# Kernel optimization log

Measured on AMD Instinct MI355X. Metric: run time of the kernel, lower is better.

## Reference

```python
import jax, jax.numpy as jnp
import numpy as np

E = 640000
N_AGENTS = 50000
D = 128
NUM_S = 50000


def setup_inputs() -> dict:
    key = jax.random.key(0)
    k1, k2, k3 = jax.random.split(key, 3)
    edge_weights = jax.random.uniform(k1, (E,), dtype=jnp.float32)
    agent_features = jax.random.normal(k2, (N_AGENTS, D), dtype=jnp.float32)
    edge_index = jax.random.randint(k3, (2, E), 0, NUM_S, dtype=jnp.int64)
    return {
        "edge_weights": edge_weights,
        "agent_features": agent_features,
        "edge_index": edge_index,
        "num_s": NUM_S,
    }


def reference(edge_weights, agent_features, edge_index, num_s):
    s_idx = edge_index[0]
    a_idx = edge_index[1]
    # gather per-edge agent features: [E, D]
    eaf = agent_features[a_idx]
    # weighted scatter-add: per-source feature sums [num_s, D] and weight sums [num_s]
    sum_wf = jax.ops.segment_sum(edge_weights[:, None] * eaf, s_idx, num_segments=num_s)
    sum_w = jax.ops.segment_sum(edge_weights, s_idx, num_segments=num_s)
    mean_per_s = sum_wf / (sum_w[:, None] + 1e-8)
    # second pass: weighted squared deviation per edge, scattered per source
    sq_diff = jnp.sum((eaf - mean_per_s[s_idx]) ** 2, axis=1)  # [E]
    var_per_s = jax.ops.segment_sum(edge_weights * sq_diff, s_idx, num_segments=num_s)
    valid = sum_w > 0
    n_valid = jnp.sum(valid)
    loss = jnp.sum(jnp.where(valid, var_per_s, 0.0)) / jnp.maximum(n_valid, 1).astype(var_per_s.dtype)
    return jnp.where(n_valid > 0, loss, jnp.asarray(0.0, var_per_s.dtype))
```

## Files before the change

### kernel.cpp

```cpp
#include <hip/hip_runtime.h>
#include <hip/hip_fp16.h>


#define D  128
#define NS 50000
#define KMAX 64
#define NBINS 391
#define BINB 512
#define CAP_PB 24

typedef unsigned long long ull;
typedef float f32x2 __attribute__((ext_vector_type(2)));


__global__ __launch_bounds__(256) void prep_bin(
    const float* __restrict__ af, unsigned char* __restrict__ af_q,
    float* __restrict__ sqnorm, float* __restrict__ accum, int* __restrict__ done,
    const int* __restrict__ s_idx, const int* __restrict__ a_idx,
    const float* __restrict__ ew,
    unsigned* __restrict__ blkCnt,
    ull* __restrict__ coarse,
    int E, int num_a)
{
    __shared__ unsigned hist[NBINS];
    const int tid = threadIdx.x;

    if (blockIdx.x < BINB) {
        const int b     = blockIdx.x;
        const int chunk = (E + BINB - 1) / BINB;
        const int e0    = b * chunk;
        const int e1    = min(E, e0 + chunk);

        for (int t = tid; t < NBINS; t += 256) hist[t] = 0;
        __syncthreads();
        for (int i = e0 + tid; i < e1; i += 256)
            atomicAdd(&hist[(unsigned)s_idx[i] >> 7], 1u);
        __syncthreads();
        for (int t = tid; t < NBINS; t += 256) {
            blkCnt[t * BINB + b] = min(hist[t], (unsigned)CAP_PB);
            hist[t] = 0;
        }
        __syncthreads();
        for (int i = e0 + tid; i < e1; i += 256) {
            int s = s_idx[i];
            unsigned bin = (unsigned)s >> 7;
            unsigned r   = atomicAdd(&hist[bin], 1u);
            if (r < CAP_PB) {
                unsigned low = ((unsigned)a_idx[i] << 16)
                             | (unsigned)__half_as_ushort(__float2half(ew[i]));
                coarse[((size_t)bin * BINB + b) * CAP_PB + r] =
                    ((ull)((unsigned)s & 127u) << 32) | (ull)low;
            }
        }
    } else {
        int pb     = blockIdx.x - BINB;
        int gtid   = pb * 256 + tid;
        int stride = ((int)gridDim.x - BINB) * 256;
        if (gtid == 0) { accum[0] = 0.f; accum[1] = 0.f; *done = 0; }

        for (int u = gtid; u < num_a * 16; u += stride) {
            int a    = u >> 4;
            int comp = (u & 15) << 3;
            const float* src = af + (size_t)a * D + comp;
            float4 v0 = *reinterpret_cast<const float4*>(src);
            float4 v1 = *reinterpret_cast<const float4*>(src + 4);
            unsigned lo = __builtin_amdgcn_cvt_pk_fp8_f32(v0.x, v0.y, 0u, false);
            lo = __builtin_amdgcn_cvt_pk_fp8_f32(v0.z, v0.w, lo, true);
            unsigned hi = __builtin_amdgcn_cvt_pk_fp8_f32(v1.x, v1.y, 0u, false);
            hi = __builtin_amdgcn_cvt_pk_fp8_f32(v1.z, v1.w, hi, true);
            int p  = comp >> 6;
            int cc = comp & 63;
            *reinterpret_cast<ull*>(af_q + ((size_t)p * num_a + a) * 64 + cc) =
                ((ull)hi << 32) | (ull)lo;

            f32x2 q0 = __builtin_amdgcn_cvt_pk_f32_fp8(lo, false);
            f32x2 q1 = __builtin_amdgcn_cvt_pk_f32_fp8(lo, true);
            f32x2 q2 = __builtin_amdgcn_cvt_pk_f32_fp8(hi, false);
            f32x2 q3 = __builtin_amdgcn_cvt_pk_f32_fp8(hi, true);
            float ss = q0.x*q0.x + q0.y*q0.y + q1.x*q1.x + q1.y*q1.y
                     + q2.x*q2.x + q2.y*q2.y + q3.x*q3.x + q3.y*q3.y;
            #pragma unroll
            for (int m = 1; m <= 8; m <<= 1) ss += __shfl_xor(ss, m, 64);
            if ((u & 15) == 0) sqnorm[a] = ss;
        }
    }
}


__global__ __launch_bounds__(256) void final_bucket(
    const ull* __restrict__ coarse,
    const unsigned* __restrict__ blkCnt,
    unsigned* __restrict__ bucket, int* __restrict__ cnt, int num_s)
{
    __shared__ unsigned lcnt[128];
    int bin = blockIdx.x;
    int tid = threadIdx.x;
    if (tid < 128) lcnt[tid] = 0;
    __syncthreads();
    for (int rr = tid; rr < BINB; rr += 256) {
        unsigned c = blkCnt[bin * BINB + rr];
        const ull* reg = coarse + ((size_t)bin * BINB + rr) * CAP_PB;
        for (unsigned r = 0; r < c; ++r) {
            ull e = reg[r];
            unsigned s7 = (unsigned)(e >> 32);
            unsigned k  = atomicAdd(&lcnt[s7], 1u);
            if (k < KMAX) {
                int s = bin * 128 + (int)s7;
                bucket[((size_t)s << 6) + k] = (unsigned)e;
            }
        }
    }
    __syncthreads();
    if (tid < 128) {
        int s = bin * 128 + tid;
        if (s < num_s) cnt[s] = (int)min(lcnt[tid], (unsigned)KMAX);
    }
}

__device__ __forceinline__ void fma16(const uint4& x, float w, float* acc) {
    f32x2 t;
    t = __builtin_amdgcn_cvt_pk_f32_fp8(x.x, false); acc[0]  += w*t.x; acc[1]  += w*t.y;
    t = __builtin_amdgcn_cvt_pk_f32_fp8(x.x, true);  acc[2]  += w*t.x; acc[3]  += w*t.y;
    t = __builtin_amdgcn_cvt_pk_f32_fp8(x.y, false); acc[4]  += w*t.x; acc[5]  += w*t.y;
    t = __builtin_amdgcn_cvt_pk_f32_fp8(x.y, true);  acc[6]  += w*t.x; acc[7]  += w*t.y;
    t = __builtin_amdgcn_cvt_pk_f32_fp8(x.z, false); acc[8]  += w*t.x; acc[9]  += w*t.y;
    t = __builtin_amdgcn_cvt_pk_f32_fp8(x.z, true);  acc[10] += w*t.x; acc[11] += w*t.y;
    t = __builtin_amdgcn_cvt_pk_f32_fp8(x.w, false); acc[12] += w*t.x; acc[13] += w*t.y;
    t = __builtin_amdgcn_cvt_pk_f32_fp8(x.w, true);  acc[14] += w*t.x; acc[15] += w*t.y;
}

__device__ __forceinline__ float decw(unsigned wa) {
    return __half2float(__ushort_as_half((unsigned short)(wa & 0xFFFFu)));
}


__global__ __launch_bounds__(256) void slice_merged(
    const unsigned char* __restrict__ af_q,
    const float* __restrict__ sqnorm,
    const unsigned* __restrict__ bucket,
    const int* __restrict__ cnt,
    float* __restrict__ fn2a, float* __restrict__ fn2b,
    float* __restrict__ s2acc, float* __restrict__ wsumv,
    int num_s, int num_a)
{
    const bool p0  = (blockIdx.x & 1u) == 0u;
    const unsigned char* afp = af_q + (p0 ? 0 : (size_t)num_a * 64);
    int lblk    = blockIdx.x >> 1;
    int gid     = lblk * 256 + threadIdx.x;
    int group   = gid >> 5;
    int lane    = threadIdx.x & 31;
    int j       = lane >> 2;
    int ccq     = lane & 3;
    int ngroups = ((gridDim.x >> 1) * 256) >> 5;

    for (int s0 = group * 2; s0 < num_s; s0 += ngroups * 2) {
        int s1 = s0 + 1;
        const unsigned* b0 = bucket + ((size_t)s0 << 6);
        const unsigned* b1 = bucket + ((size_t)s1 << 6);

        unsigned r0a = b0[j];      unsigned r0b = b0[j + 8];
        unsigned r0c = b0[j + 16]; unsigned r0d = b0[j + 24];
        unsigned r1a = b1[j];      unsigned r1b = b1[j + 8];
        unsigned r1c = b1[j + 16]; unsigned r1d = b1[j + 24];
        int2 c2 = *reinterpret_cast<const int2*>(cnt + s0);
        int c0 = min(c2.x, KMAX);
        int c1 = min(c2.y, KMAX);

        float accA[16] = {};
        float accB[16] = {};
        float s2A = 0.f, wlA = 0.f, s2B = 0.f, wlB = 0.f;

        {
            int A0a = min((int)(r0a >> 16), num_a - 1);
            int A0b = min((int)(r0b >> 16), num_a - 1);
            int A0c = min((int)(r0c >> 16), num_a - 1);
            int A0d = min((int)(r0d >> 16), num_a - 1);
            int A1a = min((int)(r1a >> 16), num_a - 1);
            int A1b = min((int)(r1b >> 16), num_a - 1);
            int A1c = min((int)(r1c >> 16), num_a - 1);
            int A1d = min((int)(r1d >> 16), num_a - 1);
            uint4 xa = *reinterpret_cast<const uint4*>(afp + ((size_t)A0a << 6) + (ccq << 4));
            uint4 xb = *reinterpret_cast<const uint4*>(afp + ((size_t)A0b << 6) + (ccq << 4));
            uint4 xc = *reinterpret_cast<const uint4*>(afp + ((size_t)A0c << 6) + (ccq << 4));
            uint4 xd = *reinterpret_cast<const uint4*>(afp + ((size_t)A0d << 6) + (ccq << 4));
            uint4 ya = *reinterpret_cast<const uint4*>(afp + ((size_t)A1a << 6) + (ccq << 4));
            uint4 yb = *reinterpret_cast<const uint4*>(afp + ((size_t)A1b << 6) + (ccq << 4));
            uint4 yc = *reinterpret_cast<const uint4*>(afp + ((size_t)A1c << 6) + (ccq << 4));
            uint4 yd = *reinterpret_cast<const uint4*>(afp + ((size_t)A1d << 6) + (ccq << 4));
            float w0a = (j      < c0) ? decw(r0a) : 0.f;
            float w0b = (j + 8  < c0) ? decw(r0b) : 0.f;
            float w0c = (j + 16 < c0) ? decw(r0c) : 0.f;
            float w0d = (j + 24 < c0) ? decw(r0d) : 0.f;
            float w1a = (j      < c1) ? decw(r1a) : 0.f;
            float w1b = (j + 8  < c1) ? decw(r1b) : 0.f;
            float w1c = (j + 16 < c1) ? decw(r1c) : 0.f;
            float w1d = (j + 24 < c1) ? decw(r1d) : 0.f;
            fma16(xa, w0a, accA); fma16(xb, w0b, accA);
            fma16(xc, w0c, accA); fma16(xd, w0d, accA);
            fma16(ya, w1a, accB); fma16(yb, w1b, accB);
            fma16(yc, w1c, accB); fma16(yd, w1d, accB);
            if (p0 && ccq == 0) {
                s2A += w0a * sqnorm[A0a] + w0b * sqnorm[A0b]
                     + w0c * sqnorm[A0c] + w0d * sqnorm[A0d];
                wlA += w0a + w0b + w0c + w0d;
                s2B += w1a * sqnorm[A1a] + w1b * sqnorm[A1b]
                     + w1c * sqnorm[A1c] + w1d * sqnorm[A1d];
                wlB += w1a + w1b + w1c + w1d;
            }
        }

        int cmax = max(c0, c1);
        if (cmax > 32) {
            int iters = (cmax + 15) >> 4;
            for (int it = 2; it < iters; ++it) {
                int idxA = it * 16 + j;
                int idxB = idxA + 8;
                unsigned wa0  = (idxA < c0) ? b0[idxA] : 0u;
                unsigned wa0b = (idxB < c0) ? b0[idxB] : 0u;
                unsigned wa1  = (idxA < c1) ? b1[idxA] : 0u;
                unsigned wa1b = (idxB < c1) ? b1[idxB] : 0u;
                float w0  = decw(wa0);
                float w0b = decw(wa0b);
                float w1  = decw(wa1);
                float w1b = decw(wa1b);
                int A0  = (int)(wa0  >> 16);
                int A0b = (int)(wa0b >> 16);
                int A1  = (int)(wa1  >> 16);
                int A1b = (int)(wa1b >> 16);
                uint4 x  = *reinterpret_cast<const uint4*>(afp + ((size_t)A0  << 6) + (ccq << 4));
                uint4 xb = *reinterpret_cast<const uint4*>(afp + ((size_t)A0b << 6) + (ccq << 4));
                uint4 y  = *reinterpret_cast<const uint4*>(afp + ((size_t)A1  << 6) + (ccq << 4));
                uint4 yb = *reinterpret_cast<const uint4*>(afp + ((size_t)A1b << 6) + (ccq << 4));
                fma16(x,  w0,  accA);
                fma16(xb, w0b, accA);
                fma16(y,  w1,  accB);
                fma16(yb, w1b, accB);
                if (p0 && ccq == 0) {
                    s2A += w0 * sqnorm[A0] + w0b * sqnorm[A0b];  wlA += w0 + w0b;
                    s2B += w1 * sqnorm[A1] + w1b * sqnorm[A1b];  wlB += w1 + w1b;
                }
            }
        }
        #pragma unroll
        for (int m = 4; m <= 16; m <<= 1) {
            #pragma unroll
            for (int k = 0; k < 16; ++k) {
                accA[k] += __shfl_xor(accA[k], m, 64);
                accB[k] += __shfl_xor(accB[k], m, 64);
            }
            if (p0) {
                s2A += __shfl_xor(s2A, m, 64); wlA += __shfl_xor(wlA, m, 64);
                s2B += __shfl_xor(s2B, m, 64); wlB += __shfl_xor(wlB, m, 64);
            }
        }
        float n2a = 0.f, n2b = 0.f;
        #pragma unroll
        for (int k = 0; k < 16; ++k) { n2a += accA[k] * accA[k]; n2b += accB[k] * accB[k]; }
        n2a += __shfl_xor(n2a, 1, 64); n2a += __shfl_xor(n2a, 2, 64);
        n2b += __shfl_xor(n2b, 1, 64); n2b += __shfl_xor(n2b, 2, 64);
        if (lane == 0) {
            if (p0) {
                fn2a[s0] = n2a;  s2acc[s0] = s2A;  wsumv[s0] = wlA;
                fn2a[s1] = n2b;  s2acc[s1] = s2B;  wsumv[s1] = wlB;
            } else {
                fn2b[s0] = n2a;
                fn2b[s1] = n2b;
            }
        }
    }
}


__global__ void loss_finalize(const float* __restrict__ fn2a, const float* __restrict__ fn2b,
                              const float* __restrict__ s2acc, const float* __restrict__ wsumv,
                              float* __restrict__ accum, int* __restrict__ done,
                              float* __restrict__ out, int num_s) {
    __shared__ float sv[4], sc[4];
    float lv = 0.f, lc = 0.f;
    for (int s = blockIdx.x * blockDim.x + threadIdx.x; s < num_s; s += gridDim.x * blockDim.x) {
        float w = wsumv[s];
        if (w > 0.f) {
            float n2  = fn2a[s] + fn2b[s];
            float inv = 1.f / (w + 1e-8f);
            lv += s2acc[s] - n2 * inv * (2.f - w * inv);
            lc += 1.f;
        }
    }
    #pragma unroll
    for (int m = 1; m < 64; m <<= 1) { lv += __shfl_xor(lv, m, 64); lc += __shfl_xor(lc, m, 64); }
    int wv = threadIdx.x >> 6;
    if ((threadIdx.x & 63) == 0) { sv[wv] = lv; sc[wv] = lc; }
    __syncthreads();
    if (threadIdx.x == 0) {
        atomicAdd(accum + 0, sv[0] + sv[1] + sv[2] + sv[3]);
        atomicAdd(accum + 1, sc[0] + sc[1] + sc[2] + sc[3]);
        __threadfence();
        unsigned t = atomicAdd((unsigned*)done, 1u);
        if (t == gridDim.x - 1) {
            float v = atomicAdd(accum + 0, 0.f);
            float c = atomicAdd(accum + 1, 0.f);
            out[0] = (c > 0.f) ? (v / fmaxf(c, 1.f)) : 0.f;
        }
    }
}

extern "C" void kernel_launch(void* const* d_in, const int* in_sizes, int n_in,
                              void* d_out, int out_size, void* d_ws, size_t ws_size,
                              hipStream_t stream) {
    const float* ew = (const float*)d_in[0];
    const float* af = (const float*)d_in[1];
    const int*   ei = (const int*)d_in[2];
    const int E     = in_sizes[0];
    const int num_a = in_sizes[1] / D;
    const int num_s = NS;

    const int* s_idx = ei;
    const int* a_idx = ei + E;

    char* ws = (char*)d_ws;
    size_t off = 0;
    auto alloc = [&](size_t bytes, size_t align) -> char* {
        off = (off + align - 1) & ~(align - 1);
        char* p = ws + off;
        off += bytes;
        return p;
    };
    float* accum  = (float*)alloc(4 * 4, 16);
    int*   done   = (int*)(accum + 2);
    int*   cnt    = (int*)alloc((size_t)num_s * 4, 16);
    float* fn2a   = (float*)alloc((size_t)num_s * 4, 16);
    float* fn2b   = (float*)alloc((size_t)num_s * 4, 16);
    float* s2acc  = (float*)alloc((size_t)num_s * 4, 16);
    float* wsumv  = (float*)alloc((size_t)num_s * 4, 16);
    float* sqnorm = (float*)alloc((size_t)num_a * 4, 16);
    unsigned* blkCnt    = (unsigned*)alloc((size_t)NBINS * BINB * 4, 64);
    unsigned char* af_q = (unsigned char*)alloc((size_t)2 * num_a * 64, 256);
    unsigned* bucket    = (unsigned*)alloc((size_t)num_s * KMAX * 4, 512);
    ull* coarse = (ull*)alloc((size_t)NBINS * BINB * CAP_PB * 8, 512);

    int prep_blocks = (num_a * 16 + 255) / 256;
    prep_bin<<<BINB + prep_blocks, 256, 0, stream>>>(af, af_q, sqnorm, accum, done,
                                                     s_idx, a_idx, ew, blkCnt, coarse,
                                                     E, num_a);
    final_bucket<<<NBINS, 256, 0, stream>>>(coarse, blkCnt, bucket, cnt, num_s);
    slice_merged<<<4096, 256, 0, stream>>>(af_q, sqnorm, bucket, cnt,
                                           fn2a, fn2b, s2acc, wsumv, num_s, num_a);
    loss_finalize<<<128, 256, 0, stream>>>(fn2a, fn2b, s2acc, wsumv, accum, done,
                                           (float*)d_out, num_s);
}
```

Measured before the change: 70.44 us.

## Fold per-source loss into slice kernel and reduce block partials in single-block finalize

The slice kernel now computes each source's loss contribution in registers instead of writing four per-source arrays. Each block writes one (value, count) partial, and a single 1024-thread block sums these partials to produce the output. This removes the per-source array traffic, the global atomics and done-counter, and the separate grid-stride finalize pass. The launch also changes from a fixed 4096-block grid-stride loop to one source pair per warp group (about 6250 blocks). Both plane halves now compute the weight sums so each can evaluate its own -n2*g term, which adds a little redundant ALU work.

New measurement: 66.78 us. -5.2%, faster.

```diff
diff --git a/kernel.cpp b/kernel.cpp
--- a/kernel.cpp
+++ b/kernel.cpp
@@ -15,7 +15,7 @@
 
 __global__ __launch_bounds__(256) void prep_bin(
     const float* __restrict__ af, unsigned char* __restrict__ af_q,
-    float* __restrict__ sqnorm, float* __restrict__ accum, int* __restrict__ done,
+    float* __restrict__ sqnorm,
     const int* __restrict__ s_idx, const int* __restrict__ a_idx,
     const float* __restrict__ ew,
     unsigned* __restrict__ blkCnt,
@@ -56,7 +56,6 @@
         int pb     = blockIdx.x - BINB;
         int gtid   = pb * 256 + tid;
         int stride = ((int)gridDim.x - BINB) * 256;
-        if (gtid == 0) { accum[0] = 0.f; accum[1] = 0.f; *done = 0; }
 
         for (int u = gtid; u < num_a * 16; u += stride) {
             int a    = u >> 4;
@@ -134,26 +133,25 @@
 }
 
 
-__global__ __launch_bounds__(256) void slice_merged(
+__global__ __launch_bounds__(256) void slice_loss(
     const unsigned char* __restrict__ af_q,
     const float* __restrict__ sqnorm,
     const unsigned* __restrict__ bucket,
     const int* __restrict__ cnt,
-    float* __restrict__ fn2a, float* __restrict__ fn2b,
-    float* __restrict__ s2acc, float* __restrict__ wsumv,
+    float2* __restrict__ partial,
     int num_s, int num_a)
 {
     const bool p0  = (blockIdx.x & 1u) == 0u;
     const unsigned char* afp = af_q + (p0 ? 0 : (size_t)num_a * 64);
-    int lblk    = blockIdx.x >> 1;
-    int gid     = lblk * 256 + threadIdx.x;
-    int group   = gid >> 5;
-    int lane    = threadIdx.x & 31;
-    int j       = lane >> 2;
-    int ccq     = lane & 3;
-    int ngroups = ((gridDim.x >> 1) * 256) >> 5;
-
-    for (int s0 = group * 2; s0 < num_s; s0 += ngroups * 2) {
+    int lblk  = blockIdx.x >> 1;
+    int group = lblk * 8 + (threadIdx.x >> 5);
+    int lane  = threadIdx.x & 31;
+    int j     = lane >> 2;
+    int ccq   = lane & 3;
+
+    float lv = 0.f, lc = 0.f;
+    int s0 = group * 2;
+    if (s0 < num_s) {
         int s1 = s0 + 1;
         const unsigned* b0 = bucket + ((size_t)s0 << 6);
         const unsigned* b1 = bucket + ((size_t)s1 << 6);
@@ -199,13 +197,15 @@
             fma16(xc, w0c, accA); fma16(xd, w0d, accA);
             fma16(ya, w1a, accB); fma16(yb, w1b, accB);
             fma16(yc, w1c, accB); fma16(yd, w1d, accB);
-            if (p0 && ccq == 0) {
-                s2A += w0a * sqnorm[A0a] + w0b * sqnorm[A0b]
-                     + w0c * sqnorm[A0c] + w0d * sqnorm[A0d];
+            if (ccq == 0) {
                 wlA += w0a + w0b + w0c + w0d;
-                s2B += w1a * sqnorm[A1a] + w1b * sqnorm[A1b]
-                     + w1c * sqnorm[A1c] + w1d * sqnorm[A1d];
                 wlB += w1a + w1b + w1c + w1d;
+                if (p0) {
+                    s2A += w0a * sqnorm[A0a] + w0b * sqnorm[A0b]
+                         + w0c * sqnorm[A0c] + w0d * sqnorm[A0d];
+                    s2B += w1a * sqnorm[A1a] + w1b * sqnorm[A1b]
+                         + w1c * sqnorm[A1c] + w1d * sqnorm[A1d];
+                }
             }
         }
 
@@ -235,9 +235,13 @@
                 fma16(xb, w0b, accA);
                 fma16(y,  w1,  accB);
                 fma16(yb, w1b, accB);
-                if (p0 && ccq == 0) {
-                    s2A += w0 * sqnorm[A0] + w0b * sqnorm[A0b];  wlA += w0 + w0b;
-                    s2B += w1 * sqnorm[A1] + w1b * sqnorm[A1b];  wlB += w1 + w1b;
+                if (ccq == 0) {
+                    wlA += w0 + w0b;
+                    wlB += w1 + w1b;
+                    if (p0) {
+                        s2A += w0 * sqnorm[A0] + w0b * sqnorm[A0b];
+                        s2B += w1 * sqnorm[A1] + w1b * sqnorm[A1b];
+                    }
                 }
             }
         }
@@ -248,9 +252,11 @@
                 accA[k] += __shfl_xor(accA[k], m, 64);
                 accB[k] += __shfl_xor(accB[k], m, 64);
             }
+            wlA += __shfl_xor(wlA, m, 64);
+            wlB += __shfl_xor(wlB, m, 64);
             if (p0) {
-                s2A += __shfl_xor(s2A, m, 64); wlA += __shfl_xor(wlA, m, 64);
-                s2B += __shfl_xor(s2B, m, 64); wlB += __shfl_xor(wlB, m, 64);
+                s2A += __shfl_xor(s2A, m, 64);
+                s2B += __shfl_xor(s2B, m, 64);
             }
         }
         float n2a = 0.f, n2b = 0.f;
@@ -259,32 +265,42 @@
         n2a += __shfl_xor(n2a, 1, 64); n2a += __shfl_xor(n2a, 2, 64);
         n2b += __shfl_xor(n2b, 1, 64); n2b += __shfl_xor(n2b, 2, 64);
         if (lane == 0) {
-            if (p0) {
-                fn2a[s0] = n2a;  s2acc[s0] = s2A;  wsumv[s0] = wlA;
-                fn2a[s1] = n2b;  s2acc[s1] = s2B;  wsumv[s1] = wlB;
-            } else {
-                fn2b[s0] = n2a;
-                fn2b[s1] = n2b;
-            }
-        }
-    }
-}
-
-
-__global__ void loss_finalize(const float* __restrict__ fn2a, const float* __restrict__ fn2b,
-                              const float* __restrict__ s2acc, const float* __restrict__ wsumv,
-                              float* __restrict__ accum, int* __restrict__ done,
-                              float* __restrict__ out, int num_s) {
-    __shared__ float sv[4], sc[4];
+            if (wlA > 0.f) {
+                float inv = 1.f / (wlA + 1e-8f);
+                float g   = inv * (2.f - wlA * inv);
+                lv += p0 ? (s2A - n2a * g) : (-n2a * g);
+                if (p0) lc += 1.f;
+            }
+            if (wlB > 0.f) {
+                float inv = 1.f / (wlB + 1e-8f);
+                float g   = inv * (2.f - wlB * inv);
+                lv += p0 ? (s2B - n2b * g) : (-n2b * g);
+                if (p0) lc += 1.f;
+            }
+        }
+    }
+
+    __shared__ float sv[8], sc[8];
+    if (lane == 0) { sv[threadIdx.x >> 5] = lv; sc[threadIdx.x >> 5] = lc; }
+    __syncthreads();
+    if (threadIdx.x == 0) {
+        float v = 0.f, c = 0.f;
+        #pragma unroll
+        for (int k = 0; k < 8; ++k) { v += sv[k]; c += sc[k]; }
+        partial[blockIdx.x] = make_float2(v, c);
+    }
+}
+
+
+__global__ __launch_bounds__(1024) void finalize_small(
+    const float2* __restrict__ partial, float* __restrict__ out, int nblk)
+{
+    __shared__ float sv[16], sc[16];
     float lv = 0.f, lc = 0.f;
-    for (int s = blockIdx.x * blockDim.x + threadIdx.x; s < num_s; s += gridDim.x * blockDim.x) {
-        float w = wsumv[s];
-        if (w > 0.f) {
-            float n2  = fn2a[s] + fn2b[s];
-            float inv = 1.f / (w + 1e-8f);
-            lv += s2acc[s] - n2 * inv * (2.f - w * inv);
-            lc += 1.f;
-        }
+    for (int i = threadIdx.x; i < nblk; i += 1024) {
+        float2 p = partial[i];
+        lv += p.x;
+        lc += p.y;
     }
     #pragma unroll
     for (int m = 1; m < 64; m <<= 1) { lv += __shfl_xor(lv, m, 64); lc += __shfl_xor(lc, m, 64); }
@@ -292,15 +308,10 @@
     if ((threadIdx.x & 63) == 0) { sv[wv] = lv; sc[wv] = lc; }
     __syncthreads();
     if (threadIdx.x == 0) {
-        atomicAdd(accum + 0, sv[0] + sv[1] + sv[2] + sv[3]);
-        atomicAdd(accum + 1, sc[0] + sc[1] + sc[2] + sc[3]);
-        __threadfence();
-        unsigned t = atomicAdd((unsigned*)done, 1u);
-        if (t == gridDim.x - 1) {
-            float v = atomicAdd(accum + 0, 0.f);
-            float c = atomicAdd(accum + 1, 0.f);
-            out[0] = (c > 0.f) ? (v / fmaxf(c, 1.f)) : 0.f;
-        }
+        float v = 0.f, c = 0.f;
+        #pragma unroll
+        for (int k = 0; k < 16; ++k) { v += sv[k]; c += sc[k]; }
+        out[0] = (c > 0.f) ? (v / fmaxf(c, 1.f)) : 0.f;
     }
 }
 
@@ -317,6 +328,10 @@
     const int* s_idx = ei;
     const int* a_idx = ei + E;
 
+    const int pairs     = num_s / 2;
+    const int blk_role  = (pairs + 7) / 8;
+    const int SLICE_BLK = blk_role * 2;
+
     char* ws = (char*)d_ws;
     size_t off = 0;
     auto alloc = [&](size_t bytes, size_t align) -> char* {
@@ -325,13 +340,8 @@
         off += bytes;
         return p;
     };
-    float* accum  = (float*)alloc(4 * 4, 16);
-    int*   done   = (int*)(accum + 2);
+    float2* partial = (float2*)alloc((size_t)SLICE_BLK * 8, 16);
     int*   cnt    = (int*)alloc((size_t)num_s * 4, 16);
-    float* fn2a   = (float*)alloc((size_t)num_s * 4, 16);
-    float* fn2b   = (float*)alloc((size_t)num_s * 4, 16);
-    float* s2acc  = (float*)alloc((size_t)num_s * 4, 16);
-    float* wsumv  = (float*)alloc((size_t)num_s * 4, 16);
     float* sqnorm = (float*)alloc((size_t)num_a * 4, 16);
     unsigned* blkCnt    = (unsigned*)alloc((size_t)NBINS * BINB * 4, 64);
     unsigned char* af_q = (unsigned char*)alloc((size_t)2 * num_a * 64, 256);
@@ -339,12 +349,11 @@
     ull* coarse = (ull*)alloc((size_t)NBINS * BINB * CAP_PB * 8, 512);
 
     int prep_blocks = (num_a * 16 + 255) / 256;
-    prep_bin<<<BINB + prep_blocks, 256, 0, stream>>>(af, af_q, sqnorm, accum, done,
+    prep_bin<<<BINB + prep_blocks, 256, 0, stream>>>(af, af_q, sqnorm,
                                                      s_idx, a_idx, ew, blkCnt, coarse,
                                                      E, num_a);
     final_bucket<<<NBINS, 256, 0, stream>>>(coarse, blkCnt, bucket, cnt, num_s);
-    slice_merged<<<4096, 256, 0, stream>>>(af_q, sqnorm, bucket, cnt,
-                                           fn2a, fn2b, s2acc, wsumv, num_s, num_a);
-    loss_finalize<<<128, 256, 0, stream>>>(fn2a, fn2b, s2acc, wsumv, accum, done,
-                                           (float*)d_out, num_s);
-}
+    slice_loss<<<SLICE_BLK, 256, 0, stream>>>(af_q, sqnorm, bucket, cnt,
+                                              partial, num_s, num_a);
+    finalize_small<<<1, 1024, 0, stream>>>(partial, (float*)d_out, SLICE_BLK);
+}
```
